# Kernel tuning notes

Hardware: AMD Instinct MI355X
Metric: run time of the kernel (lower is better)

## Reference

```python
import jax, jax.numpy as jnp
import numpy as np

N_NODES = 50000
N_EDGES = 400000
IN_DIM = 512
OUT_DIM = 512


def setup_inputs() -> dict:
    key = jax.random.key(0)
    k1, k2, k3, k4 = jax.random.split(key, 4)
    x = jax.random.normal(k1, (N_NODES, IN_DIM), dtype=jnp.float32)
    edge_index = jax.random.randint(k2, (2, N_EDGES), 0, N_NODES, dtype=jnp.int64)
    # nn.Linear(in_dim, out_dim): weight [out, in], bias [out]
    W = jax.random.normal(k3, (OUT_DIM, IN_DIM), dtype=jnp.float32) / np.sqrt(IN_DIM)
    b = jax.random.normal(k4, (OUT_DIM,), dtype=jnp.float32) * 0.01
    return {"x": x, "edge_index": edge_index, "W": W, "b": b}


def reference(x, edge_index, W, b):
    n = x.shape[0]
    loops = jnp.arange(n, dtype=edge_index.dtype)
    row = jnp.concatenate([edge_index[0], loops])  # src
    col = jnp.concatenate([edge_index[1], loops])  # dst
    # degree from row counts (matches torch.bincount(row)); self-loops ensure deg >= 1
    deg = jax.ops.segment_sum(jnp.ones(row.shape[0], dtype=x.dtype), row, num_segments=n)
    dis = jax.lax.rsqrt(deg)  # deg^-0.5
    norm = dis[row] * dis[col]  # [E+N]
    h = x @ W.T + b  # [N, out_dim]
    # out[dst] += norm * h[src], fused gather-scale-scatter
    out = jax.ops.segment_sum(norm[:, None] * h[row], col, num_segments=n)
    return jax.nn.relu(out)
```

## Files before the change

### kernel.cpp

```cpp
#include <hip/hip_runtime.h>
#include <hip/hip_bf16.h>

#define K_DIM 512
#define N_DIM 512

typedef __attribute__((ext_vector_type(8))) short s8v;
typedef __attribute__((ext_vector_type(4))) short s4v;
typedef __attribute__((ext_vector_type(4))) float f4v;

__device__ __forceinline__ short f2bf(float f) {
  union { float f; unsigned u; } v; v.f = f;
  unsigned r = (v.u + 0x7FFFu + ((v.u >> 16) & 1u)) >> 16;
  return (short)r;
}
__device__ __forceinline__ float bflo(unsigned u) {
  union { unsigned u; float f; } v; v.u = u << 16; return v.f;
}
__device__ __forceinline__ float bfhi(unsigned u) {
  union { unsigned u; float f; } v; v.u = u & 0xffff0000u; return v.f;
}

__device__ __forceinline__ void gload16(const void* g, void* l) {
  __builtin_amdgcn_global_load_lds(
      (const __attribute__((address_space(1))) void*)g,
      (__attribute__((address_space(3))) void*)l, 16, 0, 0);
}

__global__ void k_flag(const int* __restrict__ e32, int* __restrict__ flag) {
  int t = threadIdx.x;
  int v = e32[2 * t + 1];
  unsigned long long m = __ballot(v == 0);
  if (t == 0) flag[0] = (m == ~0ULL) ? 1 : 0;
}

__global__ void k_convW(const float* __restrict__ W, short* __restrict__ Wb) {
  int i = (blockIdx.x * blockDim.x + threadIdx.x) * 4;
  float4 f = *(const float4*)(W + i);
  s4v s; s[0] = f2bf(f.x); s[1] = f2bf(f.y); s[2] = f2bf(f.z); s[3] = f2bf(f.w);
  *(s4v*)(Wb + i) = s;
}

__global__ void k_convX(const float* __restrict__ x, short* __restrict__ xb,
                        long long total) {
  long long i = ((long long)blockIdx.x * 256 + threadIdx.x) * 8;
  if (i >= total) return;
  float4 f0 = *(const float4*)(x + i);
  float4 f1 = *(const float4*)(x + i + 4);
  s8v v;
  v[0] = f2bf(f0.x); v[1] = f2bf(f0.y); v[2] = f2bf(f0.z); v[3] = f2bf(f0.w);
  v[4] = f2bf(f1.x); v[5] = f2bf(f1.y); v[6] = f2bf(f1.z); v[7] = f2bf(f1.w);
  *(s8v*)(xb + i) = v;
}

__global__ void k_hist(const int* __restrict__ e32, const int* __restrict__ flag,
                       int* __restrict__ outdeg, int* __restrict__ indeg, int E) {
  int i = blockIdx.x * blockDim.x + threadIdx.x;
  if (i >= E) return;
  int st = flag[0] ? 2 : 1;
  int r = e32[(size_t)i * st];
  int c = e32[(size_t)(E + i) * st];
  atomicAdd(&outdeg[r], 1);
  atomicAdd(&indeg[c], 1);
}

__global__ void k_dis(const int* __restrict__ outdeg, float* __restrict__ dis, int n) {
  int i = blockIdx.x * blockDim.x + threadIdx.x;
  if (i < n) dis[i] = rsqrtf((float)(outdeg[i] + 1));
}

__global__ void k_scan_a(const int* __restrict__ in, int* __restrict__ part, int n) {
  __shared__ int sm[256];
  int i = blockIdx.x * 256 + threadIdx.x;
  sm[threadIdx.x] = (i < n) ? in[i] : 0;
  __syncthreads();
  for (int off = 128; off > 0; off >>= 1) {
    if (threadIdx.x < off) sm[threadIdx.x] += sm[threadIdx.x + off];
    __syncthreads();
  }
  if (threadIdx.x == 0) part[blockIdx.x] = sm[0];
}

__global__ void k_scan_b(int* __restrict__ part, int nb, int* __restrict__ row_start, int n) {
  __shared__ int sm[256];
  int t = threadIdx.x;
  int v = (t < nb) ? part[t] : 0;
  sm[t] = v; __syncthreads();
  for (int off = 1; off < 256; off <<= 1) {
    int a = (t >= off) ? sm[t - off] : 0;
    __syncthreads();
    sm[t] += a;
    __syncthreads();
  }
  part[t] = sm[t] - v;
  if (t == 255) row_start[n] = sm[255];
}

__global__ void k_scan_c(const int* __restrict__ in, const int* __restrict__ part,
                         int* __restrict__ row_start, int* __restrict__ cursor, int n) {
  __shared__ int sm[256];
  int i = blockIdx.x * 256 + threadIdx.x;
  int v = (i < n) ? in[i] : 0;
  sm[threadIdx.x] = v; __syncthreads();
  for (int off = 1; off < 256; off <<= 1) {
    int a = (threadIdx.x >= off) ? sm[threadIdx.x - off] : 0;
    __syncthreads();
    sm[threadIdx.x] += a;
    __syncthreads();
  }
  if (i < n) {
    int excl = part[blockIdx.x] + sm[threadIdx.x] - v;
    row_start[i] = excl;
    cursor[i] = excl;
  }
}

__global__ void k_fill(const int* __restrict__ e32, const int* __restrict__ flag,
                       int* __restrict__ cursor, int* __restrict__ csr, int E) {
  int i = blockIdx.x * blockDim.x + threadIdx.x;
  if (i >= E) return;
  int st = flag[0] ? 2 : 1;
  int r = e32[(size_t)i * st];
  int c = e32[(size_t)(E + i) * st];
  int p = atomicAdd(&cursor[c], 1);
  csr[p] = r;
}

__global__ __launch_bounds__(256, 3) void k_gemm(const short* __restrict__ xb,
    const short* __restrict__ Wb, const float* __restrict__ bias,
    short* __restrict__ h, int M) {
  __shared__ __align__(16) short As[2][128 * 32];
  __shared__ __align__(16) short Bs[2][128 * 32];
  int nwg = gridDim.x;
  int orig = blockIdx.x;
  int q8 = nwg >> 3, r8 = nwg & 7;
  int xcd = orig & 7, pos = orig >> 3;
  int swz = (xcd < r8 ? xcd * (q8 + 1) : r8 * (q8 + 1) + (xcd - r8) * q8) + pos;
  const int n0 = (swz & 3) * 128;
  const int m0 = (swz >> 2) * 128;

  const int tid = threadIdx.x;
  const int lane = tid & 63;
  const int wv = tid >> 6, wr = wv >> 1, wc = wv & 1;
  const int la = lane & 15, lg = lane >> 4;

  const short* ag[2];
  const short* bg[2];
  int doff[2];
  #pragma unroll
  for (int r = 0; r < 2; ++r) {
    int id = r * 256 + tid;
    int row = id >> 2;
    int ch = id & 3;
    int arow = m0 + row; if (arow >= M) arow = M - 1;
    ag[r] = xb + (size_t)arow * K_DIM + ch * 8;
    bg[r] = Wb + (size_t)(n0 + row) * K_DIM + ch * 8;
    doff[r] = (r * 256 + (tid & 192)) * 16;
  }
  int aro[4], bro[4];
  #pragma unroll
  for (int i = 0; i < 4; ++i) {
    aro[i] = (64 * wr + 16 * i + la) * 64 + lg * 16;
    bro[i] = (64 * wc + 16 * i + la) * 64 + lg * 16;
  }

  f4v acc[4][4] = {};

  #pragma unroll
  for (int r = 0; r < 2; ++r) {
    gload16(ag[r], (char*)As + doff[r]);
    gload16(bg[r], (char*)Bs + doff[r]);
  }
  __syncthreads();

  for (int kt = 0; kt < 16; ++kt) {
    const int cur = kt & 1;
    const int nxt = cur ^ 1;
    if (kt < 15) {
      const int kk = (kt + 1) * 32;
      #pragma unroll
      for (int r = 0; r < 2; ++r) {
        gload16(ag[r] + kk, (char*)As + nxt * 8192 + doff[r]);
        gload16(bg[r] + kk, (char*)Bs + nxt * 8192 + doff[r]);
      }
    }
    s8v af[4], bf[4];
    const char* ab = (const char*)As + cur * 8192;
    const char* bb = (const char*)Bs + cur * 8192;
    #pragma unroll
    for (int i = 0; i < 4; ++i) af[i] = *(const s8v*)(ab + aro[i]);
    #pragma unroll
    for (int j = 0; j < 4; ++j) bf[j] = *(const s8v*)(bb + bro[j]);
    #pragma unroll
    for (int i = 0; i < 4; ++i)
      #pragma unroll
      for (int j = 0; j < 4; ++j)
        acc[i][j] = __builtin_amdgcn_mfma_f32_16x16x32_bf16(af[i], bf[j], acc[i][j], 0, 0, 0);
    __syncthreads();
  }

  #pragma unroll
  for (int i = 0; i < 4; ++i) {
    #pragma unroll
    for (int j = 0; j < 4; ++j) {
      int col = n0 + 64 * wc + 16 * j + la;
      float bv = bias[col];
      #pragma unroll
      for (int r = 0; r < 4; ++r) {
        int row = m0 + 64 * wr + 16 * i + lg * 4 + r;
        if (row < M) h[(size_t)row * N_DIM + col] = f2bf(acc[i][j][r] + bv);
      }
    }
  }
}

__device__ __forceinline__ void acc8(float* acc, uint4 rv, float wv) {
  acc[0] += wv * bflo(rv.x); acc[1] += wv * bfhi(rv.x);
  acc[2] += wv * bflo(rv.y); acc[3] += wv * bfhi(rv.y);
  acc[4] += wv * bflo(rv.z); acc[5] += wv * bfhi(rv.z);
  acc[6] += wv * bflo(rv.w); acc[7] += wv * bfhi(rv.w);
}

__global__ __launch_bounds__(256) void k_scatter(const short* __restrict__ h,
    const float* __restrict__ dis, const int* __restrict__ row_start,
    const int* __restrict__ csr, float* __restrict__ out, int n) {
  int v = blockIdx.x * 4 + (threadIdx.x >> 6);
  if (v >= n) return;
  int lane = threadIdx.x & 63;
  const short* hl = h + lane * 8;
  float dv = dis[v];
  float acc[8];
  {
    uint4 r = *(const uint4*)(hl + (size_t)v * N_DIM);
    float w = dv * dv;
    acc[0] = w * bflo(r.x); acc[1] = w * bfhi(r.x);
    acc[2] = w * bflo(r.y); acc[3] = w * bfhi(r.y);
    acc[4] = w * bflo(r.z); acc[5] = w * bfhi(r.z);
    acc[6] = w * bflo(r.w); acc[7] = w * bfhi(r.w);
  }
  int s = __builtin_amdgcn_readfirstlane(row_start[v]);
  int e = __builtin_amdgcn_readfirstlane(row_start[v + 1]);
  int idx = s;
  for (; idx + 8 <= e; idx += 8) {
    int s0 = csr[idx],     s1 = csr[idx + 1], s2 = csr[idx + 2], s3 = csr[idx + 3];
    int s4 = csr[idx + 4], s5 = csr[idx + 5], s6 = csr[idx + 6], s7 = csr[idx + 7];
    float w0 = dis[s0] * dv, w1 = dis[s1] * dv, w2 = dis[s2] * dv, w3 = dis[s3] * dv;
    float w4 = dis[s4] * dv, w5 = dis[s5] * dv, w6 = dis[s6] * dv, w7 = dis[s7] * dv;
    uint4 r0 = *(const uint4*)(hl + (size_t)s0 * N_DIM);
    uint4 r1 = *(const uint4*)(hl + (size_t)s1 * N_DIM);
    uint4 r2 = *(const uint4*)(hl + (size_t)s2 * N_DIM);
    uint4 r3 = *(const uint4*)(hl + (size_t)s3 * N_DIM);
    uint4 r4 = *(const uint4*)(hl + (size_t)s4 * N_DIM);
    uint4 r5 = *(const uint4*)(hl + (size_t)s5 * N_DIM);
    uint4 r6 = *(const uint4*)(hl + (size_t)s6 * N_DIM);
    uint4 r7 = *(const uint4*)(hl + (size_t)s7 * N_DIM);
    acc8(acc, r0, w0); acc8(acc, r1, w1); acc8(acc, r2, w2); acc8(acc, r3, w3);
    acc8(acc, r4, w4); acc8(acc, r5, w5); acc8(acc, r6, w6); acc8(acc, r7, w7);
  }
  for (; idx + 4 <= e; idx += 4) {
    int s0 = csr[idx], s1 = csr[idx + 1], s2 = csr[idx + 2], s3 = csr[idx + 3];
    float w0 = dis[s0] * dv, w1 = dis[s1] * dv;
    float w2 = dis[s2] * dv, w3 = dis[s3] * dv;
    uint4 r0 = *(const uint4*)(hl + (size_t)s0 * N_DIM);
    uint4 r1 = *(const uint4*)(hl + (size_t)s1 * N_DIM);
    uint4 r2 = *(const uint4*)(hl + (size_t)s2 * N_DIM);
    uint4 r3 = *(const uint4*)(hl + (size_t)s3 * N_DIM);
    acc8(acc, r0, w0); acc8(acc, r1, w1); acc8(acc, r2, w2); acc8(acc, r3, w3);
  }
  for (; idx < e; ++idx) {
    int s0 = csr[idx];
    float w0 = dis[s0] * dv;
    uint4 r0 = *(const uint4*)(hl + (size_t)s0 * N_DIM);
    acc8(acc, r0, w0);
  }
  float* op = out + (size_t)v * N_DIM + lane * 8;
  float4 o0, o1;
  o0.x = fmaxf(acc[0], 0.f); o0.y = fmaxf(acc[1], 0.f);
  o0.z = fmaxf(acc[2], 0.f); o0.w = fmaxf(acc[3], 0.f);
  o1.x = fmaxf(acc[4], 0.f); o1.y = fmaxf(acc[5], 0.f);
  o1.z = fmaxf(acc[6], 0.f); o1.w = fmaxf(acc[7], 0.f);
  *(float4*)op = o0;
  *(float4*)(op + 4) = o1;
}

extern "C" void kernel_launch(void* const* d_in, const int* in_sizes, int n_in,
                              void* d_out, int out_size, void* d_ws, size_t ws_size,
                              hipStream_t stream) {
  const float* x = (const float*)d_in[0];
  const int* e32 = (const int*)d_in[1];
  const float* W = (const float*)d_in[2];
  const float* bias = (const float*)d_in[3];
  float* out = (float*)d_out;
  int M = in_sizes[0] / K_DIM;
  int E = in_sizes[1] / 2;

  char* ws = (char*)d_ws;
  size_t off = 0;
  auto alloc = [&](size_t bytes) {
    void* p = ws + off;
    off = (off + bytes + 255) & ~(size_t)255;
    return p;
  };
  short* Wb      = (short*)alloc((size_t)N_DIM * K_DIM * 2);
  short* h       = (short*)alloc((size_t)M * N_DIM * 2);
  float* dis     = (float*)alloc((size_t)M * 4);
  int*   outdeg  = (int*)alloc((size_t)M * 4);
  int*   indeg   = (int*)alloc((size_t)M * 4);
  int*   rstart  = (int*)alloc((size_t)(M + 1) * 4);
  int*   cursor  = (int*)alloc((size_t)M * 4);
  int*   part    = (int*)alloc(256 * 4);
  int*   csr     = (int*)alloc((size_t)E * 4);
  int*   flag    = (int*)alloc(4);
  if (off > ws_size) return;

  short* xb = (short*)d_out;

  (void)hipMemsetAsync(outdeg, 0, (size_t)M * 4, stream);
  (void)hipMemsetAsync(indeg, 0, (size_t)M * 4, stream);
  k_flag<<<1, 64, 0, stream>>>(e32, flag);
  k_convW<<<(N_DIM * K_DIM / 4 + 255) / 256, 256, 0, stream>>>(W, Wb);
  long long totalx = (long long)M * K_DIM;
  k_convX<<<(int)((totalx / 8 + 255) / 256), 256, 0, stream>>>(x, xb, totalx);
  k_hist<<<(E + 255) / 256, 256, 0, stream>>>(e32, flag, outdeg, indeg, E);
  k_dis<<<(M + 255) / 256, 256, 0, stream>>>(outdeg, dis, M);
  int nscan = (M + 255) / 256;
  k_scan_a<<<nscan, 256, 0, stream>>>(indeg, part, M);
  k_scan_b<<<1, 256, 0, stream>>>(part, nscan, rstart, M);
  k_scan_c<<<nscan, 256, 0, stream>>>(indeg, part, rstart, cursor, M);
  k_fill<<<(E + 255) / 256, 256, 0, stream>>>(e32, flag, cursor, csr, E);
  int nmc = (M + 127) / 128;
  k_gemm<<<nmc * 4, 256, 0, stream>>>(xb, Wb, bias, h, M);
  k_scatter<<<(M + 3) / 4, 256, 0, stream>>>(h, dis, rstart, csr, out, M);
}
```

Measured before the change: 223.6 us.

## Merge preprocessing kernels, fold source norm into GEMM epilogue, persistent scatter

Merges the flag, W/x conversion and degree histogram into one launch, and the rsqrt and partial-sum scan into another. The stride check moves inline into each kernel, so the flag buffer is no longer needed. The GEMM epilogue now pre-scales h rows by dis[src], which removes the per-edge dis gather and multiply in the scatter; the destination norm is applied once at the end. The scatter becomes a grid-stride persistent kernel with 2048 blocks and uses nontemporal stores. The cost is a rounding change, since dis is folded in before the bf16 conversion, plus some redundant ballot work per warp.

```diff
diff --git a/kernel.cpp b/kernel.cpp
--- a/kernel.cpp
+++ b/kernel.cpp
@@ -26,58 +26,64 @@
       (__attribute__((address_space(3))) void*)l, 16, 0, 0);
 }
 
-__global__ void k_flag(const int* __restrict__ e32, int* __restrict__ flag) {
+__device__ __forceinline__ int edge_stride(const int* __restrict__ e32, int lane) {
+  int chk = e32[2 * lane + 1];
+  unsigned long long m = __ballot(chk == 0);
+  return (m == ~0ULL) ? 2 : 1;
+}
+
+__global__ __launch_bounds__(256) void k_pre1(const float* __restrict__ W,
+    short* __restrict__ Wb, const float* __restrict__ x, short* __restrict__ xb,
+    long long totalx, const int* __restrict__ e32, int* __restrict__ outdeg,
+    int* __restrict__ indeg, int E, int nbw, int nbx) {
+  int b = blockIdx.x;
   int t = threadIdx.x;
-  int v = e32[2 * t + 1];
-  unsigned long long m = __ballot(v == 0);
-  if (t == 0) flag[0] = (m == ~0ULL) ? 1 : 0;
-}
-
-__global__ void k_convW(const float* __restrict__ W, short* __restrict__ Wb) {
-  int i = (blockIdx.x * blockDim.x + threadIdx.x) * 4;
-  float4 f = *(const float4*)(W + i);
-  s4v s; s[0] = f2bf(f.x); s[1] = f2bf(f.y); s[2] = f2bf(f.z); s[3] = f2bf(f.w);
-  *(s4v*)(Wb + i) = s;
-}
-
-__global__ void k_convX(const float* __restrict__ x, short* __restrict__ xb,
-                        long long total) {
-  long long i = ((long long)blockIdx.x * 256 + threadIdx.x) * 8;
-  if (i >= total) return;
-  float4 f0 = *(const float4*)(x + i);
-  float4 f1 = *(const float4*)(x + i + 4);
-  s8v v;
-  v[0] = f2bf(f0.x); v[1] = f2bf(f0.y); v[2] = f2bf(f0.z); v[3] = f2bf(f0.w);
-  v[4] = f2bf(f1.x); v[5] = f2bf(f1.y); v[6] = f2bf(f1.z); v[7] = f2bf(f1.w);
-  *(s8v*)(xb + i) = v;
-}
-
-__global__ void k_hist(const int* __restrict__ e32, const int* __restrict__ flag,
-                       int* __restrict__ outdeg, int* __restrict__ indeg, int E) {
-  int i = blockIdx.x * blockDim.x + threadIdx.x;
-  if (i >= E) return;
-  int st = flag[0] ? 2 : 1;
-  int r = e32[(size_t)i * st];
-  int c = e32[(size_t)(E + i) * st];
-  atomicAdd(&outdeg[r], 1);
-  atomicAdd(&indeg[c], 1);
-}
-
-__global__ void k_dis(const int* __restrict__ outdeg, float* __restrict__ dis, int n) {
-  int i = blockIdx.x * blockDim.x + threadIdx.x;
-  if (i < n) dis[i] = rsqrtf((float)(outdeg[i] + 1));
-}
-
-__global__ void k_scan_a(const int* __restrict__ in, int* __restrict__ part, int n) {
-  __shared__ int sm[256];
-  int i = blockIdx.x * 256 + threadIdx.x;
-  sm[threadIdx.x] = (i < n) ? in[i] : 0;
-  __syncthreads();
-  for (int off = 128; off > 0; off >>= 1) {
-    if (threadIdx.x < off) sm[threadIdx.x] += sm[threadIdx.x + off];
-    __syncthreads();
-  }
-  if (threadIdx.x == 0) part[blockIdx.x] = sm[0];
+  if (b < nbw) {
+    int i = (b * 256 + t) * 4;
+    float4 f = *(const float4*)(W + i);
+    s4v s; s[0] = f2bf(f.x); s[1] = f2bf(f.y); s[2] = f2bf(f.z); s[3] = f2bf(f.w);
+    *(s4v*)(Wb + i) = s;
+  } else if (b < nbw + nbx) {
+    long long i = ((long long)(b - nbw) * 256 + t) * 8;
+    if (i < totalx) {
+      float4 f0 = *(const float4*)(x + i);
+      float4 f1 = *(const float4*)(x + i + 4);
+      s8v v;
+      v[0] = f2bf(f0.x); v[1] = f2bf(f0.y); v[2] = f2bf(f0.z); v[3] = f2bf(f0.w);
+      v[4] = f2bf(f1.x); v[5] = f2bf(f1.y); v[6] = f2bf(f1.z); v[7] = f2bf(f1.w);
+      __builtin_nontemporal_store(v, (s8v*)(xb + i));
+    }
+  } else {
+    int st = edge_stride(e32, t & 63);
+    int i = (b - nbw - nbx) * 256 + t;
+    if (i < E) {
+      int r = e32[(size_t)i * st];
+      int c = e32[(size_t)(E + i) * st];
+      atomicAdd(&outdeg[r], 1);
+      atomicAdd(&indeg[c], 1);
+    }
+  }
+}
+
+__global__ __launch_bounds__(256) void k_pre2(const int* __restrict__ outdeg,
+    float* __restrict__ dis, const int* __restrict__ indeg, int* __restrict__ part,
+    int n, int nbd) {
+  int b = blockIdx.x;
+  if (b < nbd) {
+    int i = b * 256 + threadIdx.x;
+    if (i < n) dis[i] = rsqrtf((float)(outdeg[i] + 1));
+  } else {
+    __shared__ int sm[256];
+    int lb = b - nbd;
+    int i = lb * 256 + threadIdx.x;
+    sm[threadIdx.x] = (i < n) ? indeg[i] : 0;
+    __syncthreads();
+    for (int off = 128; off > 0; off >>= 1) {
+      if (threadIdx.x < off) sm[threadIdx.x] += sm[threadIdx.x + off];
+      __syncthreads();
+    }
+    if (threadIdx.x == 0) part[lb] = sm[0];
+  }
 }
 
 __global__ void k_scan_b(int* __restrict__ part, int nb, int* __restrict__ row_start, int n) {
@@ -114,11 +120,11 @@
   }
 }
 
-__global__ void k_fill(const int* __restrict__ e32, const int* __restrict__ flag,
-                       int* __restrict__ cursor, int* __restrict__ csr, int E) {
+__global__ void k_fill(const int* __restrict__ e32, int* __restrict__ cursor,
+                       int* __restrict__ csr, int E) {
+  int st = edge_stride(e32, threadIdx.x & 63);
   int i = blockIdx.x * blockDim.x + threadIdx.x;
   if (i >= E) return;
-  int st = flag[0] ? 2 : 1;
   int r = e32[(size_t)i * st];
   int c = e32[(size_t)(E + i) * st];
   int p = atomicAdd(&cursor[c], 1);
@@ -127,7 +133,7 @@
 
 __global__ __launch_bounds__(256, 3) void k_gemm(const short* __restrict__ xb,
     const short* __restrict__ Wb, const float* __restrict__ bias,
-    short* __restrict__ h, int M) {
+    const float* __restrict__ dis, short* __restrict__ h, int M) {
   __shared__ __align__(16) short As[2][128 * 32];
   __shared__ __align__(16) short Bs[2][128 * 32];
   int nwg = gridDim.x;
@@ -200,86 +206,86 @@
 
   #pragma unroll
   for (int i = 0; i < 4; ++i) {
+    int rowb = m0 + 64 * wr + 16 * i + lg * 4;
+    float dsv[4];
+    #pragma unroll
+    for (int r = 0; r < 4; ++r) dsv[r] = (rowb + r < M) ? dis[rowb + r] : 0.f;
     #pragma unroll
     for (int j = 0; j < 4; ++j) {
       int col = n0 + 64 * wc + 16 * j + la;
       float bv = bias[col];
       #pragma unroll
       for (int r = 0; r < 4; ++r) {
-        int row = m0 + 64 * wr + 16 * i + lg * 4 + r;
-        if (row < M) h[(size_t)row * N_DIM + col] = f2bf(acc[i][j][r] + bv);
+        if (rowb + r < M)
+          __builtin_nontemporal_store(f2bf((acc[i][j][r] + bv) * dsv[r]),
+                                      &h[(size_t)(rowb + r) * N_DIM + col]);
       }
     }
   }
 }
 
-__device__ __forceinline__ void acc8(float* acc, uint4 rv, float wv) {
-  acc[0] += wv * bflo(rv.x); acc[1] += wv * bfhi(rv.x);
-  acc[2] += wv * bflo(rv.y); acc[3] += wv * bfhi(rv.y);
-  acc[4] += wv * bflo(rv.z); acc[5] += wv * bfhi(rv.z);
-  acc[6] += wv * bflo(rv.w); acc[7] += wv * bfhi(rv.w);
+__device__ __forceinline__ void add8(float* acc, uint4 rv) {
+  acc[0] += bflo(rv.x); acc[1] += bfhi(rv.x);
+  acc[2] += bflo(rv.y); acc[3] += bfhi(rv.y);
+  acc[4] += bflo(rv.z); acc[5] += bfhi(rv.z);
+  acc[6] += bflo(rv.w); acc[7] += bfhi(rv.w);
 }
 
 __global__ __launch_bounds__(256) void k_scatter(const short* __restrict__ h,
     const float* __restrict__ dis, const int* __restrict__ row_start,
     const int* __restrict__ csr, float* __restrict__ out, int n) {
-  int v = blockIdx.x * 4 + (threadIdx.x >> 6);
-  if (v >= n) return;
+  int wid = blockIdx.x * 4 + (threadIdx.x >> 6);
+  int nw = gridDim.x * 4;
   int lane = threadIdx.x & 63;
   const short* hl = h + lane * 8;
-  float dv = dis[v];
-  float acc[8];
-  {
-    uint4 r = *(const uint4*)(hl + (size_t)v * N_DIM);
-    float w = dv * dv;
-    acc[0] = w * bflo(r.x); acc[1] = w * bfhi(r.x);
-    acc[2] = w * bflo(r.y); acc[3] = w * bfhi(r.y);
-    acc[4] = w * bflo(r.z); acc[5] = w * bfhi(r.z);
-    acc[6] = w * bflo(r.w); acc[7] = w * bfhi(r.w);
-  }
-  int s = __builtin_amdgcn_readfirstlane(row_start[v]);
-  int e = __builtin_amdgcn_readfirstlane(row_start[v + 1]);
-  int idx = s;
-  for (; idx + 8 <= e; idx += 8) {
-    int s0 = csr[idx],     s1 = csr[idx + 1], s2 = csr[idx + 2], s3 = csr[idx + 3];
-    int s4 = csr[idx + 4], s5 = csr[idx + 5], s6 = csr[idx + 6], s7 = csr[idx + 7];
-    float w0 = dis[s0] * dv, w1 = dis[s1] * dv, w2 = dis[s2] * dv, w3 = dis[s3] * dv;
-    float w4 = dis[s4] * dv, w5 = dis[s5] * dv, w6 = dis[s6] * dv, w7 = dis[s7] * dv;
-    uint4 r0 = *(const uint4*)(hl + (size_t)s0 * N_DIM);
-    uint4 r1 = *(const uint4*)(hl + (size_t)s1 * N_DIM);
-    uint4 r2 = *(const uint4*)(hl + (size_t)s2 * N_DIM);
-    uint4 r3 = *(const uint4*)(hl + (size_t)s3 * N_DIM);
-    uint4 r4 = *(const uint4*)(hl + (size_t)s4 * N_DIM);
-    uint4 r5 = *(const uint4*)(hl + (size_t)s5 * N_DIM);
-    uint4 r6 = *(const uint4*)(hl + (size_t)s6 * N_DIM);
-    uint4 r7 = *(const uint4*)(hl + (size_t)s7 * N_DIM);
-    acc8(acc, r0, w0); acc8(acc, r1, w1); acc8(acc, r2, w2); acc8(acc, r3, w3);
-    acc8(acc, r4, w4); acc8(acc, r5, w5); acc8(acc, r6, w6); acc8(acc, r7, w7);
-  }
-  for (; idx + 4 <= e; idx += 4) {
-    int s0 = csr[idx], s1 = csr[idx + 1], s2 = csr[idx + 2], s3 = csr[idx + 3];
-    float w0 = dis[s0] * dv, w1 = dis[s1] * dv;
-    float w2 = dis[s2] * dv, w3 = dis[s3] * dv;
-    uint4 r0 = *(const uint4*)(hl + (size_t)s0 * N_DIM);
-    uint4 r1 = *(const uint4*)(hl + (size_t)s1 * N_DIM);
-    uint4 r2 = *(const uint4*)(hl + (size_t)s2 * N_DIM);
-    uint4 r3 = *(const uint4*)(hl + (size_t)s3 * N_DIM);
-    acc8(acc, r0, w0); acc8(acc, r1, w1); acc8(acc, r2, w2); acc8(acc, r3, w3);
-  }
-  for (; idx < e; ++idx) {
-    int s0 = csr[idx];
-    float w0 = dis[s0] * dv;
-    uint4 r0 = *(const uint4*)(hl + (size_t)s0 * N_DIM);
-    acc8(acc, r0, w0);
-  }
-  float* op = out + (size_t)v * N_DIM + lane * 8;
-  float4 o0, o1;
-  o0.x = fmaxf(acc[0], 0.f); o0.y = fmaxf(acc[1], 0.f);
-  o0.z = fmaxf(acc[2], 0.f); o0.w = fmaxf(acc[3], 0.f);
-  o1.x = fmaxf(acc[4], 0.f); o1.y = fmaxf(acc[5], 0.f);
-  o1.z = fmaxf(acc[6], 0.f); o1.w = fmaxf(acc[7], 0.f);
-  *(float4*)op = o0;
-  *(float4*)(op + 4) = o1;
+  for (int v = wid; v < n; v += nw) {
+    float acc[8];
+    {
+      uint4 r = *(const uint4*)(hl + (size_t)v * N_DIM);
+      acc[0] = bflo(r.x); acc[1] = bfhi(r.x);
+      acc[2] = bflo(r.y); acc[3] = bfhi(r.y);
+      acc[4] = bflo(r.z); acc[5] = bfhi(r.z);
+      acc[6] = bflo(r.w); acc[7] = bfhi(r.w);
+    }
+    int s = __builtin_amdgcn_readfirstlane(row_start[v]);
+    int e = __builtin_amdgcn_readfirstlane(row_start[v + 1]);
+    int idx = s;
+    for (; idx + 8 <= e; idx += 8) {
+      int s0 = csr[idx],     s1 = csr[idx + 1], s2 = csr[idx + 2], s3 = csr[idx + 3];
+      int s4 = csr[idx + 4], s5 = csr[idx + 5], s6 = csr[idx + 6], s7 = csr[idx + 7];
+      uint4 r0 = *(const uint4*)(hl + (size_t)s0 * N_DIM);
+      uint4 r1 = *(const uint4*)(hl + (size_t)s1 * N_DIM);
+      uint4 r2 = *(const uint4*)(hl + (size_t)s2 * N_DIM);
+      uint4 r3 = *(const uint4*)(hl + (size_t)s3 * N_DIM);
+      uint4 r4 = *(const uint4*)(hl + (size_t)s4 * N_DIM);
+      uint4 r5 = *(const uint4*)(hl + (size_t)s5 * N_DIM);
+      uint4 r6 = *(const uint4*)(hl + (size_t)s6 * N_DIM);
+      uint4 r7 = *(const uint4*)(hl + (size_t)s7 * N_DIM);
+      add8(acc, r0); add8(acc, r1); add8(acc, r2); add8(acc, r3);
+      add8(acc, r4); add8(acc, r5); add8(acc, r6); add8(acc, r7);
+    }
+    for (; idx + 4 <= e; idx += 4) {
+      int s0 = csr[idx], s1 = csr[idx + 1], s2 = csr[idx + 2], s3 = csr[idx + 3];
+      uint4 r0 = *(const uint4*)(hl + (size_t)s0 * N_DIM);
+      uint4 r1 = *(const uint4*)(hl + (size_t)s1 * N_DIM);
+      uint4 r2 = *(const uint4*)(hl + (size_t)s2 * N_DIM);
+      uint4 r3 = *(const uint4*)(hl + (size_t)s3 * N_DIM);
+      add8(acc, r0); add8(acc, r1); add8(acc, r2); add8(acc, r3);
+    }
+    for (; idx < e; ++idx) {
+      uint4 r0 = *(const uint4*)(hl + (size_t)csr[idx] * N_DIM);
+      add8(acc, r0);
+    }
+    float dv = dis[v];
+    float* op = out + (size_t)v * N_DIM + lane * 8;
+    f4v o0, o1;
+    o0[0] = fmaxf(acc[0] * dv, 0.f); o0[1] = fmaxf(acc[1] * dv, 0.f);
+    o0[2] = fmaxf(acc[2] * dv, 0.f); o0[3] = fmaxf(acc[3] * dv, 0.f);
+    o1[0] = fmaxf(acc[4] * dv, 0.f); o1[1] = fmaxf(acc[5] * dv, 0.f);
+    o1[2] = fmaxf(acc[6] * dv, 0.f); o1[3] = fmaxf(acc[7] * dv, 0.f);
+    __builtin_nontemporal_store(o0, (f4v*)op);
+    __builtin_nontemporal_store(o1, (f4v*)(op + 4));
+  }
 }
 
 extern "C" void kernel_launch(void* const* d_in, const int* in_sizes, int n_in,
@@ -309,25 +315,25 @@
   int*   cursor  = (int*)alloc((size_t)M * 4);
   int*   part    = (int*)alloc(256 * 4);
   int*   csr     = (int*)alloc((size_t)E * 4);
-  int*   flag    = (int*)alloc(4);
   if (off > ws_size) return;
 
   short* xb = (short*)d_out;
 
   (void)hipMemsetAsync(outdeg, 0, (size_t)M * 4, stream);
   (void)hipMemsetAsync(indeg, 0, (size_t)M * 4, stream);
-  k_flag<<<1, 64, 0, stream>>>(e32, flag);
-  k_convW<<<(N_DIM * K_DIM / 4 + 255) / 256, 256, 0, stream>>>(W, Wb);
+
   long long totalx = (long long)M * K_DIM;
-  k_convX<<<(int)((totalx / 8 + 255) / 256), 256, 0, stream>>>(x, xb, totalx);
-  k_hist<<<(E + 255) / 256, 256, 0, stream>>>(e32, flag, outdeg, indeg, E);
-  k_dis<<<(M + 255) / 256, 256, 0, stream>>>(outdeg, dis, M);
+  int nbw = N_DIM * K_DIM / 4 / 256;
+  int nbx = (int)((totalx / 8 + 255) / 256);
+  int nbh = (E + 255) / 256;
+  k_pre1<<<nbw + nbx + nbh, 256, 0, stream>>>(W, Wb, x, xb, totalx, e32,
+                                              outdeg, indeg, E, nbw, nbx);
   int nscan = (M + 255) / 256;
-  k_scan_a<<<nscan, 256, 0, stream>>>(indeg, part, M);
+  k_pre2<<<nscan * 2, 256, 0, stream>>>(outdeg, dis, indeg, part, M, nscan);
   k_scan_b<<<1, 256, 0, stream>>>(part, nscan, rstart, M);
   k_scan_c<<<nscan, 256, 0, stream>>>(indeg, part, rstart, cursor, M);
-  k_fill<<<(E + 255) / 256, 256, 0, stream>>>(e32, flag, cursor, csr, E);
+  k_fill<<<nbh, 256, 0, stream>>>(e32, cursor, csr, E);
   int nmc = (M + 127) / 128;
-  k_gemm<<<nmc * 4, 256, 0, stream>>>(xb, Wb, bias, h, M);
-  k_scatter<<<(M + 3) / 4, 256, 0, stream>>>(h, dis, rstart, csr, out, M);
-}
+  k_gemm<<<nmc * 4, 256, 0, stream>>>(xb, Wb, bias, dis, h, M);
+  k_scatter<<<2048, 256, 0, stream>>>(h, dis, rstart, csr, out, M);
+}
```

After: 251.3 us. +12.4%, slower.
